# Kernel tuning notes

Measured on AMD Instinct MI355X. Metric: run time of the kernel, lower is better.

The kernel has to match this reference:

```python
import jax, jax.numpy as jnp
import numpy as np
from jax import lax

B, C_IN, C_MID, C_OUT, H, W = 8, 256, 128, 256, 128, 128
DN = ('NCHW', 'OIHW', 'NCHW')


def conv_bn(x, w, scale, shift, pad, relu):
    # conv (bias=False) + eval-mode BatchNorm folded to per-channel scale/shift
    y = lax.conv_general_dilated(x, w, (1, 1), [(pad, pad), (pad, pad)],
                                 dimension_numbers=DN)
    y = y * scale[None, :, None, None] + shift[None, :, None, None]
    return jax.nn.relu(y) if relu else y


def setup_inputs() -> dict:
    key = jax.random.key(0)
    ks = jax.random.split(key, 20)
    d = {"x": jax.random.normal(ks[0], (B, C_IN, H, W), dtype=jnp.float32)}
    f = 0.05  # weight scale
    def wparams(i, cout, cin, k):
        kk = jax.random.split(ks[i], 3)
        return (jax.random.normal(kk[0], (cout, cin, k, k), jnp.float32) * f,
                1.0 + 0.1 * jax.random.normal(kk[1], (cout,), jnp.float32),
                0.1 * jax.random.normal(kk[2], (cout,), jnp.float32))
    d["w_l"], d["s_l"], d["o_l"] = wparams(1, C_MID, C_IN, 3)
    d["w_r"], d["s_r"], d["o_r"] = wparams(2, C_MID, C_IN, 3)
    d["w_t"], d["s_t"], d["o_t"] = wparams(3, C_MID, C_IN, 3)
    d["w_b"], d["s_b"], d["o_b"] = wparams(4, C_MID, C_IN, 3)
    d["w2"], d["s2"], d["o2"] = wparams(5, C_OUT, C_MID, 3)
    d["w1"], d["s1"], d["o1"] = wparams(6, C_IN, C_IN, 1)
    return d


def reference(x, w_l, s_l, o_l, w_r, s_r, o_r, w_t, s_t, o_t,
              w_b, s_b, o_b, w2, s2, o2, w1, s1, o1):
    # four directional branches: conv+bn+relu then corner pooling (cummax scan)
    xl = lax.cummax(conv_bn(x, w_l, s_l, o_l, 1, True), axis=3, reverse=True)  # left: max over w'>=w
    xr = lax.cummax(conv_bn(x, w_r, s_r, o_r, 1, True), axis=3)                # right: max over w'<=w
    xt = lax.cummax(conv_bn(x, w_t, s_t, o_t, 1, True), axis=2, reverse=True)  # top: max over h'>=h
    xb = lax.cummax(conv_bn(x, w_b, s_b, o_b, 1, True), axis=2)                # bottom: max over h'<=h
    x1 = conv_bn(xl + xr + xb + xt, w2, s2, o2, 1, False)  # 3x3 conv+bn, no relu
    x2 = conv_bn(x, w1, s1, o1, 0, False)                  # 1x1 conv+bn skip, no relu
    return jax.nn.relu(x1 + x2)
```

## Files before the change

### kernel.cpp

```cpp
#include <hip/hip_runtime.h>

#define NEG_INF (-3.402823466e+38f)

typedef __bf16 bf16x8 __attribute__((ext_vector_type(8)));
typedef float  f32x16 __attribute__((ext_vector_type(16)));

__device__ __forceinline__ unsigned short f2bf(float f){
    unsigned u = __builtin_bit_cast(unsigned, f);
    u += 0x7fffu + ((u >> 16) & 1u);
    return (unsigned short)(u >> 16);
}
__device__ __forceinline__ float bf2f(unsigned short h){
    unsigned u = ((unsigned)h) << 16;
    return __builtin_bit_cast(float, u);
}

#if defined(__has_builtin)
#if __has_builtin(__builtin_amdgcn_global_load_lds)
#define ASYNC_CP 1
#endif
#endif

__device__ __forceinline__ void gl_lds(const unsigned short* g, unsigned short* lbase, int lane) {
#ifdef ASYNC_CP
    __builtin_amdgcn_global_load_lds(
        (const __attribute__((address_space(1))) unsigned int*)g,
        (__attribute__((address_space(3))) unsigned int*)lbase, 16, 0, 0);
#else
    *(uint4*)(lbase + (size_t)lane * 8) = *(const uint4*)g;
#endif
}

__global__ void __launch_bounds__(256)
k_xpose(const float* __restrict__ x, unsigned short* __restrict__ xh)
{
    __shared__ float tile[64 * 129];
    const int t = threadIdx.x;
    const int ci0 = blockIdx.x * 64, h = blockIdx.y, b = blockIdx.z;
    const float4* src = (const float4*)x;
#pragma unroll
    for (int i = 0; i < 8; ++i) {
        int idx = t + i * 256;
        int ci = idx >> 5, w4 = idx & 31;
        float4 v = src[((b * 256 + ci0 + ci) * 128 + h) * 32 + w4];
        tile[ci * 129 + w4 * 4 + 0] = v.x;
        tile[ci * 129 + w4 * 4 + 1] = v.y;
        tile[ci * 129 + w4 * 4 + 2] = v.z;
        tile[ci * 129 + w4 * 4 + 3] = v.w;
    }
    __syncthreads();
    unsigned* dst = (unsigned*)xh;
#pragma unroll
    for (int i = 0; i < 16; ++i) {
        int idx = t + i * 256;
        int w = idx >> 5, cp = idx & 31;
        float lo = tile[(cp * 2 + 0) * 129 + w];
        float hi = tile[(cp * 2 + 1) * 129 + w];
        dst[((b * 128 + h) * 128 + w) * 128 + (ci0 >> 1) + cp] =
            (unsigned)f2bf(lo) | ((unsigned)f2bf(hi) << 16);
    }
}

__global__ void __launch_bounds__(256)
k_wpack(const float* __restrict__ wl, const float* __restrict__ sl, const float* __restrict__ ol,
        const float* __restrict__ wr, const float* __restrict__ sr, const float* __restrict__ orr,
        const float* __restrict__ wt, const float* __restrict__ st, const float* __restrict__ ot,
        const float* __restrict__ wb, const float* __restrict__ sb, const float* __restrict__ ob,
        const float* __restrict__ w2, const float* __restrict__ s2, const float* __restrict__ o2,
        const float* __restrict__ w1, const float* __restrict__ s1, const float* __restrict__ o1,
        unsigned short* __restrict__ wpkBR, unsigned short* __restrict__ wpk2,
        unsigned short* __restrict__ wpk1, float* __restrict__ shF, float* __restrict__ obF)
{
    int i = blockIdx.x * 256 + threadIdx.x;
    if (i < 1179648) {
        int br = i / 294912, r = i % 294912;
        int c = r / 2304, r2 = r % 2304, ci = r2 / 9, k9 = r2 % 9;
        const float* wp = br == 0 ? wl : br == 1 ? wr : br == 2 ? wt : wb;
        const float* sp = br == 0 ? sl : br == 1 ? sr : br == 2 ? st : sb;
        float v = wp[r] * sp[c];
        int p = (c >> 4) * 64 + br * 16 + (c & 15);
        wpkBR[(((((ci >> 4) * 9 + k9) * 2 + ((ci >> 3) & 1)) * 512 + p) * 8) + (ci & 7)] = f2bf(v);
    } else if (i < 1474560) {
        int j = i - 1179648;
        int c = j / 1152, r2 = j % 1152, ci = r2 / 9, k9 = r2 % 9;
        wpk2[(((((ci >> 4) * 9 + k9) * 2 + ((ci >> 3) & 1)) * 256 + c) * 8) + (ci & 7)] = f2bf(w2[j] * s2[c]);
    } else if (i < 1540096) {
        int j = i - 1474560;
        int c = j >> 8, ci = j & 255;
        wpk1[((((ci >> 4) * 2 + ((ci >> 3) & 1)) * 256 + c) * 8) + (ci & 7)] = f2bf(w1[j] * s1[c]);
    } else if (i < 1540608) {
        int p = i - 1540096;
        int br = (p >> 4) & 3, c = (p >> 6) * 16 + (p & 15);
        const float* op = br == 0 ? ol : br == 1 ? orr : br == 2 ? ot : ob;
        shF[p] = op[c];
    } else if (i < 1540864) {
        int c = i - 1540608;
        obF[c] = o2[c] + o1[c];
    }
}

#define XIN_SH 12672
#define WBUF_SH 9216
__global__ void __launch_bounds__(256, 2)
k_brconv(const unsigned short* __restrict__ xh, const unsigned short* __restrict__ wpkBR,
         const float* __restrict__ shF, unsigned short* __restrict__ sbuf2,
         unsigned short* __restrict__ ytbT, unsigned short* __restrict__ ytbB)
{
    __shared__ __align__(16) unsigned short smem[XIN_SH + WBUF_SH + 128];
    unsigned short* xin  = smem;
    unsigned short* wbuf = smem + XIN_SH;
    float* shs = (float*)(smem + XIN_SH + WBUF_SH);

    const int t = threadIdx.x;
    const int bx = blockIdx.x, h0 = blockIdx.y << 2, b = blockIdx.z;
    const int wv = t >> 6, lane = t & 63;
    const int lo5 = lane & 31, hi1 = lane >> 5;
    const int hi32 = lane & 32;

    if (t < 64) shs[t] = shF[bx * 64 + t];
    for (int idx = t; idx < 1584; idx += 256) {
        uint4 z = make_uint4(0, 0, 0, 0);
        *(uint4*)(xin + idx * 8) = z;
    }

    f32x16 acc[2][4];
#pragma unroll
    for (int ct = 0; ct < 2; ++ct)
#pragma unroll
        for (int nb = 0; nb < 4; ++nb)
#pragma unroll
            for (int i = 0; i < 16; ++i) acc[ct][nb][i] = 0.f;

    for (int ciblk = 0; ciblk < 16; ++ciblk) {
        __syncthreads();
        for (int s = wv; s < 24; s += 4) {
            int r = s >> 2, khi = (s >> 1) & 1, half = s & 1;
            int ih = h0 - 1 + r;
            if (ih >= 0 && ih < 128) {
                const unsigned short* g = xh + (((size_t)(b * 128 + ih) * 128 + half * 64 + lane) * 256)
                                             + ciblk * 16 + khi * 8;
                unsigned short* l = xin + ((r * 2 + khi) * 132 + 1 + half * 64) * 8;
                gl_lds(g, l, lane);
            }
        }
        for (int s = wv; s < 18; s += 4) {
            const unsigned short* g = wpkBR + ((size_t)(ciblk * 18 + s) * 512 + bx * 64 + lane) * 8;
            gl_lds(g, wbuf + s * 512, lane);
        }
        __syncthreads();
#pragma unroll
        for (int k9 = 0; k9 < 9; ++k9) {
            const int kh = k9 / 3, kw = k9 % 3;
            bf16x8 a0 = *(const bf16x8*)(wbuf + ((k9 * 2 + hi1) * 64 + lo5) * 8);
            bf16x8 a1 = *(const bf16x8*)(wbuf + ((k9 * 2 + hi1) * 64 + 32 + lo5) * 8);
#pragma unroll
            for (int nb = 0; nb < 4; ++nb) {
                bf16x8 bf = *(const bf16x8*)(xin + (((wv + kh) * 2 + hi1) * 132 + nb * 32 + lo5 + kw) * 8);
                acc[0][nb] = __builtin_amdgcn_mfma_f32_32x32x16_bf16(a0, bf, acc[0][nb], 0, 0, 0);
                acc[1][nb] = __builtin_amdgcn_mfma_f32_32x32x16_bf16(a1, bf, acc[1][nb], 0, 0, 0);
            }
        }
    }
    __syncthreads();

    unsigned short* pbw = smem + wv * 3072;
    const int hg = h0 + wv;

#pragma unroll
    for (int r = 0; r < 8; ++r) {
        const int m = (r & 3) + 8 * (r >> 2) + 4 * hi1;
        const float shv = shs[m];
        float carry = NEG_INF;
#pragma unroll
        for (int nn = 3; nn >= 0; --nn) {
            float a = fmaxf(acc[0][nn][r] + shv, 0.f);
#pragma unroll
            for (int d = 1; d < 32; d <<= 1) {
                float o = __shfl_down(a, d);
                if (lo5 < 32 - d) a = fmaxf(a, o);
            }
            a = fmaxf(a, carry);
            carry = __shfl(a, hi32);
            acc[0][nn][r] = a;
        }
    }
#pragma unroll
    for (int r = 8; r < 16; ++r) {
        const int m = 16 + (r & 3) + 8 * ((r >> 2) & 1) + 4 * hi1;
        const float shv = shs[m];
        float carry = NEG_INF;
#pragma unroll
        for (int nn = 0; nn < 4; ++nn) {
            float a = fmaxf(acc[0][nn][r] + shv, 0.f);
#pragma unroll
            for (int d = 1; d < 32; d <<= 1) {
                float o = __shfl_up(a, d);
                if (lo5 >= d) a = fmaxf(a, o);
            }
            a = fmaxf(a, carry);
            carry = __shfl(a, hi32 | 31);
            acc[0][nn][r] = a;
        }
    }
#pragma unroll
    for (int r = 0; r < 8; ++r) {
        const int c16 = (r & 3) + 8 * (r >> 2) + 4 * hi1;
#pragma unroll
        for (int nn = 0; nn < 4; ++nn)
            pbw[(nn * 32 + lo5) * 24 + c16] = f2bf(acc[0][nn][r] + acc[0][nn][r + 8]);
    }
    {
        unsigned short* gdst = sbuf2 + ((size_t)(b * 128 + hg) * 128) * 128 + bx * 16;
#pragma unroll
        for (int i = 0; i < 4; ++i) {
            int idx = lane + i * 64;
            int w = idx >> 1, part = idx & 1;
            *(uint4*)(gdst + (size_t)w * 128 + part * 8) = *(const uint4*)(pbw + w * 24 + part * 8);
        }
    }
#pragma unroll
    for (int r = 0; r < 8; ++r) {
        const int c16 = (r & 3) + 8 * (r >> 2) + 4 * hi1;
        const float shv = shs[32 + c16];
#pragma unroll
        for (int nn = 0; nn < 4; ++nn)
            pbw[(nn * 32 + lo5) * 24 + c16] = f2bf(fmaxf(acc[1][nn][r] + shv, 0.f));
    }
    {
        unsigned short* gdst = ytbT + ((size_t)(b * 128 + hg) * 128) * 128 + bx * 16;
#pragma unroll
        for (int i = 0; i < 4; ++i) {
            int idx = lane + i * 64;
            int w = idx >> 1, part = idx & 1;
            *(uint4*)(gdst + (size_t)w * 128 + part * 8) = *(const uint4*)(pbw + w * 24 + part * 8);
        }
    }
#pragma unroll
    for (int r = 8; r < 16; ++r) {
        const int c16 = (r & 3) + 8 * ((r >> 2) & 1) + 4 * hi1;
        const float shv = shs[48 + c16];
#pragma unroll
        for (int nn = 0; nn < 4; ++nn)
            pbw[(nn * 32 + lo5) * 24 + c16] = f2bf(fmaxf(acc[1][nn][r] + shv, 0.f));
    }
    {
        unsigned short* gdst = ytbB + ((size_t)(b * 128 + hg) * 128) * 128 + bx * 16;
#pragma unroll
        for (int i = 0; i < 4; ++i) {
            int idx = lane + i * 64;
            int w = idx >> 1, part = idx & 1;
            *(uint4*)(gdst + (size_t)w * 128 + part * 8) = *(const uint4*)(pbw + w * 24 + part * 8);
        }
    }
}

template<int REV>
__global__ void __launch_bounds__(256)
k_colscan(const unsigned short* __restrict__ ytb, unsigned short* __restrict__ sbuf2)
{
    __shared__ float tile[8][8][33];
    const int t = threadIdx.x;
    const int w0 = blockIdx.x * 8, c0 = blockIdx.y * 32, b = blockIdx.z;
    const int sc = t & 31, sw = t >> 5;
    const int rh = t >> 5, r5 = t & 31;
    const int rw = r5 >> 2, rcq = r5 & 3;
    float cum = NEG_INF;
    for (int step = 0; step < 16; ++step) {
        int h0 = REV ? 120 - step * 8 : step * 8;
        for (int q = 0; q < 8; ++q) {
            int hh = REV ? 7 - q : q;
            int hg = h0 + hh;
            float v = bf2f(ytb[((b * 128 + hg) * 128 + (w0 + sw)) * 128 + c0 + sc]);
            cum = fmaxf(cum, v);
            tile[hh][sw][sc] = cum;
        }
        __syncthreads();
        {
            int hg = h0 + rh;
            unsigned short* p = sbuf2 + ((b * 128 + hg) * 128 + w0 + rw) * 128 + c0 + rcq * 8;
            uint4 u = *(uint4*)p;
            unsigned short* us = (unsigned short*)&u;
#pragma unroll
            for (int j = 0; j < 8; ++j)
                us[j] = f2bf(bf2f(us[j]) + tile[rh][rw][rcq * 8 + j]);
            *(uint4*)p = u;
        }
        __syncthreads();
    }
}

__global__ void __launch_bounds__(256, 2)
k_final(const unsigned short* __restrict__ sbuf2, const unsigned short* __restrict__ xh,
        const unsigned short* __restrict__ wpk2, const unsigned short* __restrict__ wpk1,
        const float* __restrict__ obF, float* __restrict__ out)
{
    __shared__ __align__(16) unsigned short smem[XIN_SH + WBUF_SH + 128];
    unsigned short* xin  = smem;
    unsigned short* wbuf = smem + XIN_SH;
    float* obs = (float*)(smem + XIN_SH + WBUF_SH);

    const int t = threadIdx.x;
    const int bx = blockIdx.x, h0 = blockIdx.y << 2, b = blockIdx.z;
    const int wv = t >> 6, lane = t & 63;
    const int lo5 = lane & 31, hi1 = lane >> 5;

    if (t < 64) obs[t] = obF[bx * 64 + t];
    for (int idx = t; idx < 1584; idx += 256) {
        uint4 z = make_uint4(0, 0, 0, 0);
        *(uint4*)(xin + idx * 8) = z;
    }

    f32x16 acc[2][4];
#pragma unroll
    for (int ct = 0; ct < 2; ++ct)
#pragma unroll
        for (int nb = 0; nb < 4; ++nb)
#pragma unroll
            for (int i = 0; i < 16; ++i) acc[ct][nb][i] = 0.f;

    for (int ciblk = 0; ciblk < 8; ++ciblk) {
        __syncthreads();
        for (int s = wv; s < 24; s += 4) {
            int r = s >> 2, khi = (s >> 1) & 1, half = s & 1;
            int ih = h0 - 1 + r;
            if (ih >= 0 && ih < 128) {
                const unsigned short* g = sbuf2 + (((size_t)(b * 128 + ih) * 128 + half * 64 + lane) * 128)
                                                 + ciblk * 16 + khi * 8;
                unsigned short* l = xin + ((r * 2 + khi) * 132 + 1 + half * 64) * 8;
                gl_lds(g, l, lane);
            }
        }
        for (int s = wv; s < 18; s += 4) {
            const unsigned short* g = wpk2 + ((size_t)(ciblk * 18 + s) * 256 + bx * 64 + lane) * 8;
            gl_lds(g, wbuf + s * 512, lane);
        }
        __syncthreads();
#pragma unroll
        for (int k9 = 0; k9 < 9; ++k9) {
            const int kh = k9 / 3, kw = k9 % 3;
            bf16x8 a0 = *(const bf16x8*)(wbuf + ((k9 * 2 + hi1) * 64 + lo5) * 8);
            bf16x8 a1 = *(const bf16x8*)(wbuf + ((k9 * 2 + hi1) * 64 + 32 + lo5) * 8);
#pragma unroll
            for (int nb = 0; nb < 4; ++nb) {
                bf16x8 bf = *(const bf16x8*)(xin + (((wv + kh) * 2 + hi1) * 132 + nb * 32 + lo5 + kw) * 8);
                acc[0][nb] = __builtin_amdgcn_mfma_f32_32x32x16_bf16(a0, bf, acc[0][nb], 0, 0, 0);
                acc[1][nb] = __builtin_amdgcn_mfma_f32_32x32x16_bf16(a1, bf, acc[1][nb], 0, 0, 0);
            }
        }
    }
    for (int ciblk = 0; ciblk < 16; ++ciblk) {
        __syncthreads();
        for (int s = wv; s < 16; s += 4) {
            int wr = s >> 2, khi = (s >> 1) & 1, half = s & 1;
            int ih = h0 + wr;
            const unsigned short* g = xh + (((size_t)(b * 128 + ih) * 128 + half * 64 + lane) * 256)
                                         + ciblk * 16 + khi * 8;
            unsigned short* l = xin + ((wr * 2 + khi) * 132 + 1 + half * 64) * 8;
            gl_lds(g, l, lane);
        }
        for (int s = wv; s < 2; s += 4) {
            const unsigned short* g = wpk1 + ((size_t)(ciblk * 2 + s) * 256 + bx * 64 + lane) * 8;
            gl_lds(g, wbuf + s * 512, lane);
        }
        __syncthreads();
        {
            bf16x8 a0 = *(const bf16x8*)(wbuf + (hi1 * 64 + lo5) * 8);
            bf16x8 a1 = *(const bf16x8*)(wbuf + (hi1 * 64 + 32 + lo5) * 8);
#pragma unroll
            for (int nb = 0; nb < 4; ++nb) {
                bf16x8 bf = *(const bf16x8*)(xin + ((wv * 2 + hi1) * 132 + 1 + nb * 32 + lo5) * 8);
                acc[0][nb] = __builtin_amdgcn_mfma_f32_32x32x16_bf16(a0, bf, acc[0][nb], 0, 0, 0);
                acc[1][nb] = __builtin_amdgcn_mfma_f32_32x32x16_bf16(a1, bf, acc[1][nb], 0, 0, 0);
            }
        }
    }
    __syncthreads();

    const int hg = h0 + wv;
#pragma unroll
    for (int ct = 0; ct < 2; ++ct)
#pragma unroll
        for (int r = 0; r < 16; ++r) {
            const int m = ct * 32 + (r & 3) + 8 * (r >> 2) + 4 * hi1;
            const float bias = obs[m];
#pragma unroll
            for (int nb = 0; nb < 4; ++nb)
                out[((size_t)(b * 256 + bx * 64 + m) * 128 + hg) * 128 + nb * 32 + lo5] =
                    fmaxf(acc[ct][nb][r] + bias, 0.f);
        }
}

extern "C" void kernel_launch(void* const* d_in, const int* in_sizes, int n_in,
                              void* d_out, int out_size, void* d_ws, size_t ws_size,
                              hipStream_t stream)
{
    const float* x   = (const float*)d_in[0];
    const float* w_l = (const float*)d_in[1];
    const float* s_l = (const float*)d_in[2];
    const float* o_l = (const float*)d_in[3];
    const float* w_r = (const float*)d_in[4];
    const float* s_r = (const float*)d_in[5];
    const float* o_r = (const float*)d_in[6];
    const float* w_t = (const float*)d_in[7];
    const float* s_t = (const float*)d_in[8];
    const float* o_t = (const float*)d_in[9];
    const float* w_b = (const float*)d_in[10];
    const float* s_b = (const float*)d_in[11];
    const float* o_b = (const float*)d_in[12];
    const float* w2  = (const float*)d_in[13];
    const float* s2  = (const float*)d_in[14];
    const float* o2  = (const float*)d_in[15];
    const float* w1  = (const float*)d_in[16];
    const float* s1  = (const float*)d_in[17];
    const float* o1  = (const float*)d_in[18];
    float* out = (float*)d_out;
    char*  ws  = (char*)d_ws;

    unsigned short* xh    = (unsigned short*)(ws + 0);
    unsigned short* sbuf2 = (unsigned short*)(ws + 67108864);
    unsigned short* wpkBR = (unsigned short*)(ws + 100663296);
    unsigned short* wpk2  = (unsigned short*)(ws + 103022592);
    unsigned short* wpk1  = (unsigned short*)(ws + 103612416);
    float* shF = (float*)(ws + 103743488);
    float* obF = (float*)(ws + 103745536);

    unsigned short* ytbT = (unsigned short*)d_out;
    unsigned short* ytbB = ytbT + 16777216;

    dim3 blk(256);
    k_xpose<<<dim3(4, 128, 8), blk, 0, stream>>>(x, xh);
    k_wpack<<<dim3(6019), blk, 0, stream>>>(w_l, s_l, o_l, w_r, s_r, o_r,
                                            w_t, s_t, o_t, w_b, s_b, o_b,
                                            w2, s2, o2, w1, s1, o1,
                                            wpkBR, wpk2, wpk1, shF, obF);
    k_brconv<<<dim3(8, 32, 8), blk, 0, stream>>>(xh, wpkBR, shF, sbuf2, ytbT, ytbB);
    k_colscan<1><<<dim3(16, 4, 8), blk, 0, stream>>>(ytbT, sbuf2);
    k_colscan<0><<<dim3(16, 4, 8), blk, 0, stream>>>(ytbB, sbuf2);
    k_final<<<dim3(4, 32, 8), blk, 0, stream>>>(sbuf2, xh, wpk2, wpk1, obF, out);
}
```

Baseline: 790.1 us.

## Double-buffer input tiles and register-prefetch weights in conv kernels; swizzle block order

```diff
diff --git a/kernel.cpp b/kernel.cpp
--- a/kernel.cpp
+++ b/kernel.cpp
@@ -106,22 +106,23 @@
          const float* __restrict__ shF, unsigned short* __restrict__ sbuf2,
          unsigned short* __restrict__ ytbT, unsigned short* __restrict__ ytbB)
 {
-    __shared__ __align__(16) unsigned short smem[XIN_SH + WBUF_SH + 128];
-    unsigned short* xin  = smem;
-    unsigned short* wbuf = smem + XIN_SH;
-    float* shs = (float*)(smem + XIN_SH + WBUF_SH);
+    __shared__ __align__(16) unsigned short smem[2 * XIN_SH + WBUF_SH + 128];
+    unsigned short* xinA = smem;
+    unsigned short* xinB = smem + XIN_SH;
+    unsigned short* wbuf = smem + 2 * XIN_SH;
+    float* shs = (float*)(smem + 2 * XIN_SH + WBUF_SH);
 
     const int t = threadIdx.x;
-    const int bx = blockIdx.x, h0 = blockIdx.y << 2, b = blockIdx.z;
+    const int lin = (int)blockIdx.x + ((int)blockIdx.y << 3) + ((int)blockIdx.z << 8);
+    const int swz = (lin & 7) * 256 + (lin >> 3);
+    const int bx = swz & 7, h0 = ((swz >> 3) & 31) << 2, b = swz >> 8;
     const int wv = t >> 6, lane = t & 63;
     const int lo5 = lane & 31, hi1 = lane >> 5;
     const int hi32 = lane & 32;
 
     if (t < 64) shs[t] = shF[bx * 64 + t];
-    for (int idx = t; idx < 1584; idx += 256) {
-        uint4 z = make_uint4(0, 0, 0, 0);
-        *(uint4*)(xin + idx * 8) = z;
-    }
+    for (int idx = t; idx < 3168; idx += 256)
+        *(uint4*)(smem + idx * 8) = make_uint4(0, 0, 0, 0);
 
     f32x16 acc[2][4];
 #pragma unroll
@@ -131,23 +132,40 @@
 #pragma unroll
             for (int i = 0; i < 16; ++i) acc[ct][nb][i] = 0.f;
 
-    for (int ciblk = 0; ciblk < 16; ++ciblk) {
-        __syncthreads();
-        for (int s = wv; s < 24; s += 4) {
-            int r = s >> 2, khi = (s >> 1) & 1, half = s & 1;
-            int ih = h0 - 1 + r;
-            if (ih >= 0 && ih < 128) {
-                const unsigned short* g = xh + (((size_t)(b * 128 + ih) * 128 + half * 64 + lane) * 256)
-                                             + ciblk * 16 + khi * 8;
-                unsigned short* l = xin + ((r * 2 + khi) * 132 + 1 + half * 64) * 8;
-                gl_lds(g, l, lane);
-            }
-        }
-        for (int s = wv; s < 18; s += 4) {
-            const unsigned short* g = wpkBR + ((size_t)(ciblk * 18 + s) * 512 + bx * 64 + lane) * 8;
-            gl_lds(g, wbuf + s * 512, lane);
-        }
-        __syncthreads();
+    __syncthreads();
+
+    for (int s = wv; s < 24; s += 4) {
+        int r = s >> 2, khi = (s >> 1) & 1, half = s & 1;
+        int ih = h0 - 1 + r;
+        if (ih >= 0 && ih < 128)
+            gl_lds(xh + (((size_t)(b * 128 + ih) * 128 + half * 64 + lane) * 256) + khi * 8,
+                   xinA + ((r * 2 + khi) * 132 + 1 + half * 64) * 8, lane);
+    }
+    for (int s = wv; s < 18; s += 4)
+        gl_lds(wpkBR + ((size_t)s * 512 + bx * 64 + lane) * 8, wbuf + s * 512, lane);
+    __syncthreads();
+
+    uint4 wr0 = make_uint4(0, 0, 0, 0), wr1 = wr0, wr2 = wr0, wr3 = wr0, wr4 = wr0;
+    unsigned short* xcur = xinA;
+    unsigned short* xnxt = xinB;
+
+    for (int cb = 0; cb < 16; ++cb) {
+        if (cb < 15) {
+            const int nc = cb + 1;
+            for (int s = wv; s < 24; s += 4) {
+                int r = s >> 2, khi = (s >> 1) & 1, half = s & 1;
+                int ih = h0 - 1 + r;
+                if (ih >= 0 && ih < 128)
+                    gl_lds(xh + (((size_t)(b * 128 + ih) * 128 + half * 64 + lane) * 256) + nc * 16 + khi * 8,
+                           xnxt + ((r * 2 + khi) * 132 + 1 + half * 64) * 8, lane);
+            }
+            wr0 = *(const uint4*)(wpkBR + ((size_t)(nc * 18 + wv) * 512 + bx * 64 + lane) * 8);
+            wr1 = *(const uint4*)(wpkBR + ((size_t)(nc * 18 + wv + 4) * 512 + bx * 64 + lane) * 8);
+            wr2 = *(const uint4*)(wpkBR + ((size_t)(nc * 18 + wv + 8) * 512 + bx * 64 + lane) * 8);
+            wr3 = *(const uint4*)(wpkBR + ((size_t)(nc * 18 + wv + 12) * 512 + bx * 64 + lane) * 8);
+            if (wv < 2)
+                wr4 = *(const uint4*)(wpkBR + ((size_t)(nc * 18 + wv + 16) * 512 + bx * 64 + lane) * 8);
+        }
 #pragma unroll
         for (int k9 = 0; k9 < 9; ++k9) {
             const int kh = k9 / 3, kw = k9 % 3;
@@ -155,13 +173,23 @@
             bf16x8 a1 = *(const bf16x8*)(wbuf + ((k9 * 2 + hi1) * 64 + 32 + lo5) * 8);
 #pragma unroll
             for (int nb = 0; nb < 4; ++nb) {
-                bf16x8 bf = *(const bf16x8*)(xin + (((wv + kh) * 2 + hi1) * 132 + nb * 32 + lo5 + kw) * 8);
+                bf16x8 bf = *(const bf16x8*)(xcur + (((wv + kh) * 2 + hi1) * 132 + nb * 32 + lo5 + kw) * 8);
                 acc[0][nb] = __builtin_amdgcn_mfma_f32_32x32x16_bf16(a0, bf, acc[0][nb], 0, 0, 0);
                 acc[1][nb] = __builtin_amdgcn_mfma_f32_32x32x16_bf16(a1, bf, acc[1][nb], 0, 0, 0);
             }
         }
-    }
-    __syncthreads();
+        __syncthreads();
+        if (cb < 15) {
+            *(uint4*)(wbuf + (wv) * 512 + lane * 8) = wr0;
+            *(uint4*)(wbuf + (wv + 4) * 512 + lane * 8) = wr1;
+            *(uint4*)(wbuf + (wv + 8) * 512 + lane * 8) = wr2;
+            *(uint4*)(wbuf + (wv + 12) * 512 + lane * 8) = wr3;
+            if (wv < 2)
+                *(uint4*)(wbuf + (wv + 16) * 512 + lane * 8) = wr4;
+            __syncthreads();
+            unsigned short* tp = xcur; xcur = xnxt; xnxt = tp;
+        }
+    }
 
     unsigned short* pbw = smem + wv * 3072;
     const int hg = h0 + wv;
@@ -294,21 +322,22 @@
         const unsigned short* __restrict__ wpk2, const unsigned short* __restrict__ wpk1,
         const float* __restrict__ obF, float* __restrict__ out)
 {
-    __shared__ __align__(16) unsigned short smem[XIN_SH + WBUF_SH + 128];
-    unsigned short* xin  = smem;
-    unsigned short* wbuf = smem + XIN_SH;
-    float* obs = (float*)(smem + XIN_SH + WBUF_SH);
+    __shared__ __align__(16) unsigned short smem[2 * XIN_SH + WBUF_SH + 128];
+    unsigned short* xinA = smem;
+    unsigned short* xinB = smem + XIN_SH;
+    unsigned short* wbuf = smem + 2 * XIN_SH;
+    float* obs = (float*)(smem + 2 * XIN_SH + WBUF_SH);
 
     const int t = threadIdx.x;
-    const int bx = blockIdx.x, h0 = blockIdx.y << 2, b = blockIdx.z;
+    const int lin = (int)blockIdx.x + ((int)blockIdx.y << 2) + ((int)blockIdx.z << 7);
+    const int swz = (lin & 7) * 128 + (lin >> 3);
+    const int bx = swz & 3, h0 = ((swz >> 2) & 31) << 2, b = swz >> 7;
     const int wv = t >> 6, lane = t & 63;
     const int lo5 = lane & 31, hi1 = lane >> 5;
 
     if (t < 64) obs[t] = obF[bx * 64 + t];
-    for (int idx = t; idx < 1584; idx += 256) {
-        uint4 z = make_uint4(0, 0, 0, 0);
-        *(uint4*)(xin + idx * 8) = z;
-    }
+    for (int idx = t; idx < 3168; idx += 256)
+        *(uint4*)(smem + idx * 8) = make_uint4(0, 0, 0, 0);
 
     f32x16 acc[2][4];
 #pragma unroll
@@ -318,23 +347,40 @@
 #pragma unroll
             for (int i = 0; i < 16; ++i) acc[ct][nb][i] = 0.f;
 
-    for (int ciblk = 0; ciblk < 8; ++ciblk) {
-        __syncthreads();
-        for (int s = wv; s < 24; s += 4) {
-            int r = s >> 2, khi = (s >> 1) & 1, half = s & 1;
-            int ih = h0 - 1 + r;
-            if (ih >= 0 && ih < 128) {
-                const unsigned short* g = sbuf2 + (((size_t)(b * 128 + ih) * 128 + half * 64 + lane) * 128)
-                                                 + ciblk * 16 + khi * 8;
-                unsigned short* l = xin + ((r * 2 + khi) * 132 + 1 + half * 64) * 8;
-                gl_lds(g, l, lane);
-            }
-        }
-        for (int s = wv; s < 18; s += 4) {
-            const unsigned short* g = wpk2 + ((size_t)(ciblk * 18 + s) * 256 + bx * 64 + lane) * 8;
-            gl_lds(g, wbuf + s * 512, lane);
-        }
-        __syncthreads();
+    __syncthreads();
+
+    for (int s = wv; s < 24; s += 4) {
+        int r = s >> 2, khi = (s >> 1) & 1, half = s & 1;
+        int ih = h0 - 1 + r;
+        if (ih >= 0 && ih < 128)
+            gl_lds(sbuf2 + (((size_t)(b * 128 + ih) * 128 + half * 64 + lane) * 128) + khi * 8,
+                   xinA + ((r * 2 + khi) * 132 + 1 + half * 64) * 8, lane);
+    }
+    for (int s = wv; s < 18; s += 4)
+        gl_lds(wpk2 + ((size_t)s * 256 + bx * 64 + lane) * 8, wbuf + s * 512, lane);
+    __syncthreads();
+
+    uint4 wr0 = make_uint4(0, 0, 0, 0), wr1 = wr0, wr2 = wr0, wr3 = wr0, wr4 = wr0;
+    unsigned short* xcur = xinA;
+    unsigned short* xnxt = xinB;
+
+    for (int cb = 0; cb < 8; ++cb) {
+        if (cb < 7) {
+            const int nc = cb + 1;
+            for (int s = wv; s < 24; s += 4) {
+                int r = s >> 2, khi = (s >> 1) & 1, half = s & 1;
+                int ih = h0 - 1 + r;
+                if (ih >= 0 && ih < 128)
+                    gl_lds(sbuf2 + (((size_t)(b * 128 + ih) * 128 + half * 64 + lane) * 128) + nc * 16 + khi * 8,
+                           xnxt + ((r * 2 + khi) * 132 + 1 + half * 64) * 8, lane);
+            }
+            wr0 = *(const uint4*)(wpk2 + ((size_t)(nc * 18 + wv) * 256 + bx * 64 + lane) * 8);
+            wr1 = *(const uint4*)(wpk2 + ((size_t)(nc * 18 + wv + 4) * 256 + bx * 64 + lane) * 8);
+            wr2 = *(const uint4*)(wpk2 + ((size_t)(nc * 18 + wv + 8) * 256 + bx * 64 + lane) * 8);
+            wr3 = *(const uint4*)(wpk2 + ((size_t)(nc * 18 + wv + 12) * 256 + bx * 64 + lane) * 8);
+            if (wv < 2)
+                wr4 = *(const uint4*)(wpk2 + ((size_t)(nc * 18 + wv + 16) * 256 + bx * 64 + lane) * 8);
+        }
 #pragma unroll
         for (int k9 = 0; k9 < 9; ++k9) {
             const int kh = k9 / 3, kw = k9 % 3;
@@ -342,39 +388,64 @@
             bf16x8 a1 = *(const bf16x8*)(wbuf + ((k9 * 2 + hi1) * 64 + 32 + lo5) * 8);
 #pragma unroll
             for (int nb = 0; nb < 4; ++nb) {
-                bf16x8 bf = *(const bf16x8*)(xin + (((wv + kh) * 2 + hi1) * 132 + nb * 32 + lo5 + kw) * 8);
+                bf16x8 bf = *(const bf16x8*)(xcur + (((wv + kh) * 2 + hi1) * 132 + nb * 32 + lo5 + kw) * 8);
                 acc[0][nb] = __builtin_amdgcn_mfma_f32_32x32x16_bf16(a0, bf, acc[0][nb], 0, 0, 0);
                 acc[1][nb] = __builtin_amdgcn_mfma_f32_32x32x16_bf16(a1, bf, acc[1][nb], 0, 0, 0);
             }
         }
-    }
-    for (int ciblk = 0; ciblk < 16; ++ciblk) {
         __syncthreads();
-        for (int s = wv; s < 16; s += 4) {
-            int wr = s >> 2, khi = (s >> 1) & 1, half = s & 1;
-            int ih = h0 + wr;
-            const unsigned short* g = xh + (((size_t)(b * 128 + ih) * 128 + half * 64 + lane) * 256)
-                                         + ciblk * 16 + khi * 8;
-            unsigned short* l = xin + ((wr * 2 + khi) * 132 + 1 + half * 64) * 8;
-            gl_lds(g, l, lane);
-        }
-        for (int s = wv; s < 2; s += 4) {
-            const unsigned short* g = wpk1 + ((size_t)(ciblk * 2 + s) * 256 + bx * 64 + lane) * 8;
-            gl_lds(g, wbuf + s * 512, lane);
-        }
-        __syncthreads();
+        if (cb < 7) {
+            *(uint4*)(wbuf + (wv) * 512 + lane * 8) = wr0;
+            *(uint4*)(wbuf + (wv + 4) * 512 + lane * 8) = wr1;
+            *(uint4*)(wbuf + (wv + 8) * 512 + lane * 8) = wr2;
+            *(uint4*)(wbuf + (wv + 12) * 512 + lane * 8) = wr3;
+            if (wv < 2)
+                *(uint4*)(wbuf + (wv + 16) * 512 + lane * 8) = wr4;
+            __syncthreads();
+            unsigned short* tp = xcur; xcur = xnxt; xnxt = tp;
+        }
+    }
+
+    for (int s = wv; s < 16; s += 4) {
+        int wr_ = s >> 2, khi = (s >> 1) & 1, half = s & 1;
+        int ih = h0 + wr_;
+        gl_lds(xh + (((size_t)(b * 128 + ih) * 128 + half * 64 + lane) * 256) + khi * 8,
+               xnxt + ((wr_ * 2 + khi) * 132 + 1 + half * 64) * 8, lane);
+    }
+    for (int s = wv; s < 2; s += 4)
+        gl_lds(wpk1 + ((size_t)s * 256 + bx * 64 + lane) * 8, wbuf + s * 512, lane);
+    __syncthreads();
+    { unsigned short* tp = xcur; xcur = xnxt; xnxt = tp; }
+
+    for (int cb = 0; cb < 16; ++cb) {
+        if (cb < 15) {
+            const int nc = cb + 1;
+            for (int s = wv; s < 16; s += 4) {
+                int wr_ = s >> 2, khi = (s >> 1) & 1, half = s & 1;
+                int ih = h0 + wr_;
+                gl_lds(xh + (((size_t)(b * 128 + ih) * 128 + half * 64 + lane) * 256) + nc * 16 + khi * 8,
+                       xnxt + ((wr_ * 2 + khi) * 132 + 1 + half * 64) * 8, lane);
+            }
+            if (wv < 2)
+                wr0 = *(const uint4*)(wpk1 + ((size_t)(nc * 2 + wv) * 256 + bx * 64 + lane) * 8);
+        }
         {
             bf16x8 a0 = *(const bf16x8*)(wbuf + (hi1 * 64 + lo5) * 8);
             bf16x8 a1 = *(const bf16x8*)(wbuf + (hi1 * 64 + 32 + lo5) * 8);
 #pragma unroll
             for (int nb = 0; nb < 4; ++nb) {
-                bf16x8 bf = *(const bf16x8*)(xin + ((wv * 2 + hi1) * 132 + 1 + nb * 32 + lo5) * 8);
+                bf16x8 bf = *(const bf16x8*)(xcur + ((wv * 2 + hi1) * 132 + 1 + nb * 32 + lo5) * 8);
                 acc[0][nb] = __builtin_amdgcn_mfma_f32_32x32x16_bf16(a0, bf, acc[0][nb], 0, 0, 0);
                 acc[1][nb] = __builtin_amdgcn_mfma_f32_32x32x16_bf16(a1, bf, acc[1][nb], 0, 0, 0);
             }
         }
-    }
-    __syncthreads();
+        __syncthreads();
+        if (cb < 15) {
+            if (wv < 2) *(uint4*)(wbuf + wv * 512 + lane * 8) = wr0;
+            __syncthreads();
+            unsigned short* tp = xcur; xcur = xnxt; xnxt = tp;
+        }
+    }
 
     const int hg = h0 + wv;
 #pragma unroll
```

Measured after the change: 692.0 us. 12.4% less time.
